# Kernel optimization log

Hardware: AMD Instinct MI355X
Metric: run time of the kernel (lower is better)

Reference implementation:

```python
import math
import jax, jax.numpy as jnp
import numpy as np

N_IMAGES = 32
TOTAL_Q = 2048
TOTAL_KV = 2048
Q_IN = 1024
KV_IN = Q_IN + 9
D_QK = 1024
D_V = 1024
N_HEADS = 16
TEMP = 1.0
SCALER = 1.0 / (TEMP * math.sqrt(D_QK // N_HEADS))


def _ragged_seg_ids(total, n_seg, seed):
    rng = np.random.default_rng(seed)
    lens = rng.multinomial(total - n_seg, np.ones(n_seg) / n_seg) + 1  # every segment nonempty
    return jnp.asarray(np.repeat(np.arange(n_seg), lens), dtype=jnp.int32)


def setup_inputs() -> dict:
    key = jax.random.key(0)
    ks = jax.random.split(key, 12)
    s = 0.02
    return {
        "A": jax.random.normal(ks[0], (TOTAL_Q, Q_IN), jnp.float32),
        "B0": jax.random.normal(ks[1], (TOTAL_KV, KV_IN), jnp.float32),
        "seg_q": _ragged_seg_ids(TOTAL_Q, N_IMAGES, 1),
        "seg_kv": _ragged_seg_ids(TOTAL_KV, N_IMAGES, 2),
        "Wq": jax.random.normal(ks[2], (Q_IN, D_QK), jnp.float32) * s,
        "bq": jax.random.normal(ks[3], (D_QK,), jnp.float32) * s,
        "Wk": jax.random.normal(ks[4], (KV_IN, D_QK), jnp.float32) * s,
        "bk": jax.random.normal(ks[5], (D_QK,), jnp.float32) * s,
        "Wv": jax.random.normal(ks[6], (KV_IN, D_V), jnp.float32) * s,
        "bv": jax.random.normal(ks[7], (D_V,), jnp.float32) * s,
        "Wf": jax.random.normal(ks[8], (D_V, Q_IN), jnp.float32) * s,
        "bf": jax.random.normal(ks[9], (Q_IN,), jnp.float32) * s,
    }


def reference(A, B0, seg_q, seg_kv, Wq, bq, Wk, bk, Wv, bv, Wf, bf):
    # Linear projections on packed rows
    q = (A @ Wq + bq).reshape(TOTAL_Q, N_HEADS, -1)     # [Nq, h, dqk]
    k = (B0 @ Wk + bk).reshape(TOTAL_KV, N_HEADS, -1)   # [Nk, h, dqk]
    v = (B0 @ Wv + bv).reshape(TOTAL_KV, N_HEADS, -1)   # [Nk, h, dv]
    # Per-segment attention expressed as a block mask (same math as the
    # original Python loop over splits)
    scores = jnp.einsum('ihd,khd->ihk', q, k) * SCALER  # [Nq, h, Nk]
    mask = (seg_q[:, None] == seg_kv[None, :])[:, None, :]  # [Nq, 1, Nk]
    neg = jnp.finfo(scores.dtype).min
    w = jax.nn.softmax(jnp.where(mask, scores, neg), axis=-1)
    wv = jnp.einsum('ihk,khd->ihd', w, v).reshape(TOTAL_Q, -1)  # [Nq, h*dv]
    return wv @ Wf + bf  # [Nq, q_in_dim]
```

## Files before the change

### kernel.cpp

```cpp
#include <hip/hip_runtime.h>
#include <hip/hip_bf16.h>
#include <math.h>

#define TOTAL_Q   2048
#define TOTAL_KV  2048
#define QIN       1024
#define KVIN      1033
#define KVIN_P    1056
#define DQK       1024
#define DV        1024
#define KVSTR     2048
#define SCALER    0.125f

typedef __bf16 bf16x8 __attribute__((ext_vector_type(8)));
typedef float  f32x4  __attribute__((ext_vector_type(4)));

__device__ __forceinline__ void glds16(const __hip_bfloat16* g, __bf16* l)
{
    __builtin_amdgcn_global_load_lds(
        (const __attribute__((address_space(1))) void*)g,
        (__attribute__((address_space(3))) void*)l,
        16, 0, 0);
}

__global__ __launch_bounds__(256)
void cast_bf16_k(const float* __restrict__ in, __hip_bfloat16* __restrict__ out, int n)
{
    int i = (blockIdx.x * 256 + threadIdx.x) * 4;
    if (i >= n) return;
    float4 f = *(const float4*)(in + i);
    __hip_bfloat16 o[4] = { __float2bfloat16(f.x), __float2bfloat16(f.y),
                            __float2bfloat16(f.z), __float2bfloat16(f.w) };
    *(uint2*)(out + i) = *(const uint2*)o;
}

__global__ __launch_bounds__(256)
void cast_pad_k(const float* __restrict__ in, __hip_bfloat16* __restrict__ out)
{
    int idx = blockIdx.x * 256 + threadIdx.x;
    if (idx >= TOTAL_KV * KVIN_P) return;
    int r = idx / KVIN_P, c = idx - r * KVIN_P;
    float v = (c < KVIN) ? in[(size_t)r * KVIN + c] : 0.f;
    out[idx] = __float2bfloat16(v);
}

__global__ __launch_bounds__(256)
void transpose_cast2_k(const float* __restrict__ W0, const float* __restrict__ W1,
                       __hip_bfloat16* __restrict__ D0, __hip_bfloat16* __restrict__ D1,
                       int K, int Kp)
{
    const float* W = blockIdx.z ? W1 : W0;
    __hip_bfloat16* Wt = blockIdx.z ? D1 : D0;
    __shared__ float tile[32][33];
    const int k0 = blockIdx.x * 32, n0 = blockIdx.y * 32;
    #pragma unroll
    for (int i = 0; i < 4; ++i) {
        int k = k0 + threadIdx.y + i * 8;
        tile[threadIdx.y + i * 8][threadIdx.x] =
            (k < K) ? W[(size_t)k * 1024 + n0 + threadIdx.x] : 0.f;
    }
    __syncthreads();
    #pragma unroll
    for (int i = 0; i < 4; ++i) {
        int n = n0 + threadIdx.y + i * 8;
        Wt[(size_t)n * Kp + k0 + threadIdx.x] =
            __float2bfloat16(tile[threadIdx.x][threadIdx.y + i * 8]);
    }
}

template<int OUT_BF16>
__global__ __launch_bounds__(256)
void gemm_glds(const __hip_bfloat16* __restrict__ A,
               const __hip_bfloat16* __restrict__ Bt,
               const float* __restrict__ biasA, const float* __restrict__ biasB,
               int nsplit,
               void* __restrict__ Cv,
               int M, int N, int K)
{
    __shared__ __bf16 As[128 * 32];
    __shared__ __bf16 Bs[64 * 32];

    const int tid  = threadIdx.x;
    const int wave = tid >> 6, lane = tid & 63;
    const int quad = lane >> 4, l16 = lane & 15;
    const int wm = (wave >> 1) * 64;
    const int wn = (wave & 1) * 32;
    const int row0 = blockIdx.y * 128, col0 = blockIdx.x * 64;

    const int cr = lane >> 2;
    const int cc = (lane & 3) * 8;

    const __hip_bfloat16* ga0 = A  + (size_t)(row0 + (wave * 2 + 0) * 16 + cr) * K + cc;
    const __hip_bfloat16* ga1 = A  + (size_t)(row0 + (wave * 2 + 1) * 16 + cr) * K + cc;
    const __hip_bfloat16* gb0 = Bt + (size_t)(col0 + wave * 16 + cr) * K + cc;

    f32x4 acc[4][2] = {};

    for (int k0 = 0; k0 < K; k0 += 32) {
        glds16(ga0 + k0, &As[(wave * 2 + 0) * 512]);
        glds16(ga1 + k0, &As[(wave * 2 + 1) * 512]);
        glds16(gb0 + k0, &Bs[wave * 512]);
        __syncthreads();

        bf16x8 af[4], bfr[2];
        #pragma unroll
        for (int mi = 0; mi < 4; ++mi)
            af[mi] = *(const bf16x8*)&As[(wm + mi * 16 + l16) * 32 + quad * 8];
        #pragma unroll
        for (int ni = 0; ni < 2; ++ni)
            bfr[ni] = *(const bf16x8*)&Bs[(wn + ni * 16 + l16) * 32 + quad * 8];

        #pragma unroll
        for (int mi = 0; mi < 4; ++mi)
            #pragma unroll
            for (int ni = 0; ni < 2; ++ni)
                acc[mi][ni] = __builtin_amdgcn_mfma_f32_16x16x32_bf16(
                    af[mi], bfr[ni], acc[mi][ni], 0, 0, 0);
        __syncthreads();
    }

    #pragma unroll
    for (int mi = 0; mi < 4; ++mi) {
        #pragma unroll
        for (int ni = 0; ni < 2; ++ni) {
            const int col = col0 + wn + ni * 16 + l16;
            const float b = (col < nsplit) ? biasA[col] : biasB[col - nsplit];
            #pragma unroll
            for (int r = 0; r < 4; ++r) {
                const int row = row0 + wm + mi * 16 + quad * 4 + r;
                const float val = acc[mi][ni][r] + b;
                if (OUT_BF16)
                    ((__hip_bfloat16*)Cv)[(size_t)row * N + col] = __float2bfloat16(val);
                else
                    ((float*)Cv)[(size_t)row * N + col] = val;
            }
        }
    }
}

#define CH 64

__global__ __launch_bounds__(256)
void attn_mfma(const __hip_bfloat16* __restrict__ qg,
               const __hip_bfloat16* __restrict__ kg,
               const __hip_bfloat16* __restrict__ vg,
               const int* __restrict__ seg_q, const int* __restrict__ seg_kv,
               __hip_bfloat16* __restrict__ wv)
{
    const int h = blockIdx.x & 15;
    const int s = blockIdx.x >> 4;

    __shared__ int sb[4];
    __shared__ __bf16 Ks[CH][72];
    __shared__ __bf16 Vt[64][CH + 8];
    __shared__ __bf16 Ps[4][16][CH + 8];

    if (threadIdx.x == 0) {
        int lo, hi;
        lo = 0; hi = TOTAL_Q;
        while (lo < hi) { int m = (lo + hi) >> 1; if (seg_q[m] <  s) lo = m + 1; else hi = m; }
        sb[0] = lo;
        hi = TOTAL_Q;
        while (lo < hi) { int m = (lo + hi) >> 1; if (seg_q[m] <= s) lo = m + 1; else hi = m; }
        sb[1] = lo;
        lo = 0; hi = TOTAL_KV;
        while (lo < hi) { int m = (lo + hi) >> 1; if (seg_kv[m] <  s) lo = m + 1; else hi = m; }
        sb[2] = lo;
        hi = TOTAL_KV;
        while (lo < hi) { int m = (lo + hi) >> 1; if (seg_kv[m] <= s) lo = m + 1; else hi = m; }
        sb[3] = lo;
    }
    __syncthreads();
    const int qbeg = sb[0], qend = sb[1], kbeg = sb[2], kend = sb[3];

    const int tid  = threadIdx.x;
    const int wave = tid >> 6, lane = tid & 63;
    const int quad = lane >> 4, l16 = lane & 15;

    for (int qt = qbeg; qt < qend; qt += 64) {
        const int qrow = qt + wave * 16 + l16;
        const int qrc  = min(qrow, qend - 1);
        bf16x8 qf[2];
        qf[0] = *(const bf16x8*)(qg + (size_t)qrc * DQK + h * 64 + quad * 8);
        qf[1] = *(const bf16x8*)(qg + (size_t)qrc * DQK + h * 64 + 32 + quad * 8);

        float m[4]  = { -1e30f, -1e30f, -1e30f, -1e30f };
        float l[4]  = { 0.f, 0.f, 0.f, 0.f };
        f32x4 acc[4] = {};

        for (int c0 = kbeg; c0 < kend; c0 += CH) {
            const int cl = min(CH, kend - c0);
            __syncthreads();

            #pragma unroll
            for (int it = 0; it < 2; ++it) {
                int e = (it * 256 + tid) * 8;
                int r = e >> 6, d = e & 63;
                bf16x8 z = {};
                if (r < cl)
                    z = *(const bf16x8*)(kg + (size_t)(c0 + r) * KVSTR + h * 64 + d);
                *(bf16x8*)&Ks[r][d] = z;
            }
            #pragma unroll
            for (int it = 0; it < 4; ++it) {
                int e = (it * 256 + tid) * 4;
                int r = e >> 6, d = e & 63;
                __bf16 t0 = 0, t1 = 0, t2 = 0, t3 = 0;
                if (r < cl) {
                    bf16x8 vv;
                    uint2 uu = *(const uint2*)(vg + (size_t)(c0 + r) * KVSTR + h * 64 + d);
                    *(uint2*)&vv = uu;
                    t0 = vv[0]; t1 = vv[1]; t2 = vv[2]; t3 = vv[3];
                }
                Vt[d + 0][r] = t0; Vt[d + 1][r] = t1;
                Vt[d + 2][r] = t2; Vt[d + 3][r] = t3;
            }
            __syncthreads();

            f32x4 sc[4];
            #pragma unroll
            for (int t = 0; t < 4; ++t) {
                bf16x8 b0 = *(const bf16x8*)&Ks[t * 16 + l16][quad * 8];
                bf16x8 b1 = *(const bf16x8*)&Ks[t * 16 + l16][32 + quad * 8];
                f32x4 z = {};
                z = __builtin_amdgcn_mfma_f32_16x16x32_bf16(qf[0], b0, z, 0, 0, 0);
                z = __builtin_amdgcn_mfma_f32_16x16x32_bf16(qf[1], b1, z, 0, 0, 0);
                sc[t] = z;
            }

            float sv[4][4];
            #pragma unroll
            for (int t = 0; t < 4; ++t) {
                const bool ok = (c0 + t * 16 + l16) < kend;
                #pragma unroll
                for (int r = 0; r < 4; ++r)
                    sv[t][r] = ok ? sc[t][r] * SCALER : -1e30f;
            }

            #pragma unroll
            for (int r = 0; r < 4; ++r) {
                float mx = fmaxf(fmaxf(sv[0][r], sv[1][r]), fmaxf(sv[2][r], sv[3][r]));
                mx = fmaxf(mx, __shfl_xor(mx, 1));
                mx = fmaxf(mx, __shfl_xor(mx, 2));
                mx = fmaxf(mx, __shfl_xor(mx, 4));
                mx = fmaxf(mx, __shfl_xor(mx, 8));
                const float mn = fmaxf(m[r], mx);
                const float alpha = __expf(m[r] - mn);
                m[r] = mn;
                float rs = 0.f;
                #pragma unroll
                for (int t = 0; t < 4; ++t) {
                    const float p = __expf(sv[t][r] - mn);
                    sv[t][r] = p;
                    rs += p;
                }
                rs += __shfl_xor(rs, 1);
                rs += __shfl_xor(rs, 2);
                rs += __shfl_xor(rs, 4);
                rs += __shfl_xor(rs, 8);
                l[r] = l[r] * alpha + rs;
                #pragma unroll
                for (int dt = 0; dt < 4; ++dt) acc[dt][r] *= alpha;
            }

            #pragma unroll
            for (int t = 0; t < 4; ++t)
                #pragma unroll
                for (int r = 0; r < 4; ++r)
                    Ps[wave][quad * 4 + r][t * 16 + l16] = (__bf16)sv[t][r];
            __syncthreads();

            #pragma unroll
            for (int ks = 0; ks < 2; ++ks) {
                bf16x8 pa = *(const bf16x8*)&Ps[wave][l16][ks * 32 + quad * 8];
                #pragma unroll
                for (int dt = 0; dt < 4; ++dt) {
                    bf16x8 vbf = *(const bf16x8*)&Vt[dt * 16 + l16][ks * 32 + quad * 8];
                    acc[dt] = __builtin_amdgcn_mfma_f32_16x16x32_bf16(pa, vbf, acc[dt], 0, 0, 0);
                }
            }
        }

        float inv[4];
        #pragma unroll
        for (int r = 0; r < 4; ++r) inv[r] = 1.f / l[r];
        #pragma unroll
        for (int dt = 0; dt < 4; ++dt) {
            #pragma unroll
            for (int r = 0; r < 4; ++r) {
                const int row = qt + wave * 16 + quad * 4 + r;
                if (row < qend)
                    wv[(size_t)row * DV + h * 64 + dt * 16 + l16] =
                        __float2bfloat16(acc[dt][r] * inv[r]);
            }
        }
    }
}

extern "C" void kernel_launch(void* const* d_in, const int* in_sizes, int n_in,
                              void* d_out, int out_size, void* d_ws, size_t ws_size,
                              hipStream_t stream)
{
    const float* A     = (const float*)d_in[0];
    const float* B0    = (const float*)d_in[1];
    const int*   seg_q = (const int*)  d_in[2];
    const int*   seg_kv= (const int*)  d_in[3];
    const float* Wq    = (const float*)d_in[4];
    const float* bq    = (const float*)d_in[5];
    const float* Wk    = (const float*)d_in[6];
    const float* bk    = (const float*)d_in[7];
    const float* Wv    = (const float*)d_in[8];
    const float* bv    = (const float*)d_in[9];
    const float* Wf    = (const float*)d_in[10];
    const float* bf    = (const float*)d_in[11];
    float* out = (float*)d_out;

    __hip_bfloat16* B0bf = (__hip_bfloat16*)d_ws;
    __hip_bfloat16* Wqt  = B0bf + (size_t)TOTAL_KV * KVIN_P;
    __hip_bfloat16* Wkt  = Wqt  + (size_t)QIN * DQK;
    __hip_bfloat16* Wvt  = Wkt  + (size_t)DQK * KVIN_P;
    __hip_bfloat16* Wft  = Wvt  + (size_t)DV * KVIN_P;
    __hip_bfloat16* Abf  = Wft  + (size_t)DV * QIN;
    __hip_bfloat16* qb   = Abf  + (size_t)TOTAL_Q * QIN;
    __hip_bfloat16* kvb  = qb   + (size_t)TOTAL_Q * DQK;
    __hip_bfloat16* wvb  = Abf;

    const dim3 b256(256);

    cast_bf16_k<<<dim3((TOTAL_Q * QIN / 4 + 255) / 256), b256, 0, stream>>>(A, Abf, TOTAL_Q * QIN);
    cast_pad_k<<<dim3((TOTAL_KV * KVIN_P + 255) / 256), b256, 0, stream>>>(B0, B0bf);
    transpose_cast2_k<<<dim3(DQK / 32, 1024 / 32, 2), dim3(32, 8), 0, stream>>>(
        Wq, Wf, Wqt, Wft, QIN, DQK);
    transpose_cast2_k<<<dim3(KVIN_P / 32, 1024 / 32, 2), dim3(32, 8), 0, stream>>>(
        Wk, Wv, Wkt, Wvt, KVIN, KVIN_P);

    gemm_glds<1><<<dim3(DQK / 64, TOTAL_Q / 128), b256, 0, stream>>>(
        Abf, Wqt, bq, bq, DQK, qb, TOTAL_Q, DQK, QIN);
    gemm_glds<1><<<dim3(KVSTR / 64, TOTAL_KV / 128), b256, 0, stream>>>(
        B0bf, Wkt, bk, bv, 1024, kvb, TOTAL_KV, KVSTR, KVIN_P);

    attn_mfma<<<dim3(32 * 16), b256, 0, stream>>>(qb, kvb, kvb + 1024, seg_q, seg_kv, wvb);

    gemm_glds<0><<<dim3(QIN / 64, TOTAL_Q / 128), b256, 0, stream>>>(
        wvb, Wft, bf, bf, QIN, out, TOTAL_Q, QIN, DV);
}
```

Measured before the change: 185.0 us.

## Fuse preprocessing kernels into one launch and merge Q/KV GEMMs with larger tiles

Merges the four cast/transpose kernels into a single prep kernel that dispatches on block index, and folds the Q and KV projection GEMMs into one launch. The merged GEMM uses 128x128 tiles instead of 128x64, so each block reuses more data per load. The B0 cast now writes four elements per thread. This cuts launch overhead and tail gaps between small kernels, but the larger tiles mean fewer blocks (384) and more accumulator registers per thread, which may lower occupancy.

Result: faster. 173.5 us (-6.2%).

```diff
diff --git a/kernel.cpp b/kernel.cpp
--- a/kernel.cpp
+++ b/kernel.cpp
@@ -24,58 +24,160 @@
 }
 
 __global__ __launch_bounds__(256)
-void cast_bf16_k(const float* __restrict__ in, __hip_bfloat16* __restrict__ out, int n)
-{
-    int i = (blockIdx.x * 256 + threadIdx.x) * 4;
-    if (i >= n) return;
-    float4 f = *(const float4*)(in + i);
-    __hip_bfloat16 o[4] = { __float2bfloat16(f.x), __float2bfloat16(f.y),
-                            __float2bfloat16(f.z), __float2bfloat16(f.w) };
-    *(uint2*)(out + i) = *(const uint2*)o;
-}
-
-__global__ __launch_bounds__(256)
-void cast_pad_k(const float* __restrict__ in, __hip_bfloat16* __restrict__ out)
-{
-    int idx = blockIdx.x * 256 + threadIdx.x;
-    if (idx >= TOTAL_KV * KVIN_P) return;
-    int r = idx / KVIN_P, c = idx - r * KVIN_P;
-    float v = (c < KVIN) ? in[(size_t)r * KVIN + c] : 0.f;
-    out[idx] = __float2bfloat16(v);
-}
-
-__global__ __launch_bounds__(256)
-void transpose_cast2_k(const float* __restrict__ W0, const float* __restrict__ W1,
-                       __hip_bfloat16* __restrict__ D0, __hip_bfloat16* __restrict__ D1,
-                       int K, int Kp)
-{
-    const float* W = blockIdx.z ? W1 : W0;
-    __hip_bfloat16* Wt = blockIdx.z ? D1 : D0;
+void prep_k(const float* __restrict__ A,  const float* __restrict__ B0,
+            const float* __restrict__ Wq, const float* __restrict__ Wk,
+            const float* __restrict__ Wv, const float* __restrict__ Wf,
+            __hip_bfloat16* __restrict__ Abf, __hip_bfloat16* __restrict__ B0bf,
+            __hip_bfloat16* __restrict__ Wqt, __hip_bfloat16* __restrict__ Wkt,
+            __hip_bfloat16* __restrict__ Wvt, __hip_bfloat16* __restrict__ Wft)
+{
+    const int b   = blockIdx.x;
+    const int tid = threadIdx.x;
+
+    if (b < 2048) {
+        int i = (b * 256 + tid) * 4;
+        float4 f = *(const float4*)(A + i);
+        __hip_bfloat16 o[4] = { __float2bfloat16(f.x), __float2bfloat16(f.y),
+                                __float2bfloat16(f.z), __float2bfloat16(f.w) };
+        *(uint2*)(Abf + i) = *(const uint2*)o;
+        return;
+    }
+    if (b < 4160) {
+        int idx = ((b - 2048) * 256 + tid) * 4;
+        int r = idx / KVIN_P, c = idx - r * KVIN_P;
+        __hip_bfloat16 o[4];
+        #pragma unroll
+        for (int j = 0; j < 4; ++j)
+            o[j] = __float2bfloat16((c + j < KVIN) ? B0[(size_t)r * KVIN + c + j] : 0.f);
+        *(uint2*)(B0bf + idx) = *(const uint2*)o;
+        return;
+    }
+
+    const float* W; __hip_bfloat16* Wt; int K, Kp, k0, n0;
+    if (b < 6208) {
+        int z = b - 4160;
+        W  = (z >= 1024) ? Wf : Wq;
+        Wt = (z >= 1024) ? Wft : Wqt;
+        K = 1024; Kp = 1024;
+        int rem = z & 1023;
+        k0 = (rem & 31) * 32; n0 = (rem >> 5) * 32;
+    } else {
+        int z = b - 6208;
+        W  = (z >= 1056) ? Wv : Wk;
+        Wt = (z >= 1056) ? Wvt : Wkt;
+        K = KVIN; Kp = KVIN_P;
+        int rem = (z >= 1056) ? z - 1056 : z;
+        k0 = (rem % 33) * 32; n0 = (rem / 33) * 32;
+    }
+    const int tx = tid & 31, ty = tid >> 5;
     __shared__ float tile[32][33];
-    const int k0 = blockIdx.x * 32, n0 = blockIdx.y * 32;
     #pragma unroll
     for (int i = 0; i < 4; ++i) {
-        int k = k0 + threadIdx.y + i * 8;
-        tile[threadIdx.y + i * 8][threadIdx.x] =
-            (k < K) ? W[(size_t)k * 1024 + n0 + threadIdx.x] : 0.f;
+        int k = k0 + ty + i * 8;
+        tile[ty + i * 8][tx] = (k < K) ? W[(size_t)k * 1024 + n0 + tx] : 0.f;
     }
     __syncthreads();
     #pragma unroll
     for (int i = 0; i < 4; ++i) {
-        int n = n0 + threadIdx.y + i * 8;
-        Wt[(size_t)n * Kp + k0 + threadIdx.x] =
-            __float2bfloat16(tile[threadIdx.x][threadIdx.y + i * 8]);
-    }
-}
-
-template<int OUT_BF16>
+        int n = n0 + ty + i * 8;
+        Wt[(size_t)n * Kp + k0 + tx] = __float2bfloat16(tile[tx][ty + i * 8]);
+    }
+}
+
 __global__ __launch_bounds__(256)
-void gemm_glds(const __hip_bfloat16* __restrict__ A,
-               const __hip_bfloat16* __restrict__ Bt,
-               const float* __restrict__ biasA, const float* __restrict__ biasB,
-               int nsplit,
-               void* __restrict__ Cv,
-               int M, int N, int K)
+void gemm_qkv(const __hip_bfloat16* __restrict__ Abf,
+              const __hip_bfloat16* __restrict__ Wqt,
+              const float* __restrict__ bq,
+              __hip_bfloat16* __restrict__ qb,
+              const __hip_bfloat16* __restrict__ B0bf,
+              const __hip_bfloat16* __restrict__ Wkvt,
+              const float* __restrict__ bk, const float* __restrict__ bv,
+              __hip_bfloat16* __restrict__ kvb)
+{
+    __shared__ __bf16 As[128 * 32];
+    __shared__ __bf16 Bs[128 * 32];
+
+    int b = blockIdx.x;
+    const __hip_bfloat16 *Ag, *Btg; const float *bias0, *bias1;
+    __hip_bfloat16* C; int N, K, bx, by;
+    if (b < 128) {
+        Ag = Abf; Btg = Wqt; bias0 = bq; bias1 = bq; C = qb;
+        N = 1024; K = 1024; bx = b & 7; by = b >> 3;
+    } else {
+        b -= 128;
+        Ag = B0bf; Btg = Wkvt; bias0 = bk; bias1 = bv; C = kvb;
+        N = 2048; K = KVIN_P; bx = b & 15; by = b >> 4;
+    }
+    const int row0 = by * 128, col0 = bx * 128;
+
+    const int tid  = threadIdx.x;
+    const int wave = tid >> 6, lane = tid & 63;
+    const int quad = lane >> 4, l16 = lane & 15;
+    const int wm = (wave >> 1) * 64, wn = (wave & 1) * 64;
+
+    const int cr = lane >> 2;
+    const int cc = (lane & 3) * 8;
+
+    const __hip_bfloat16* gsrc[4];
+    __bf16* ldst[4];
+    #pragma unroll
+    for (int i = 0; i < 4; ++i) {
+        int c = wave * 4 + i;
+        if (c < 8) {
+            gsrc[i] = Ag  + (size_t)(row0 + c * 16 + cr) * K + cc;
+            ldst[i] = &As[c * 512];
+        } else {
+            gsrc[i] = Btg + (size_t)(col0 + (c - 8) * 16 + cr) * K + cc;
+            ldst[i] = &Bs[(c - 8) * 512];
+        }
+    }
+
+    f32x4 acc[4][4] = {};
+
+    for (int k0 = 0; k0 < K; k0 += 32) {
+        #pragma unroll
+        for (int i = 0; i < 4; ++i)
+            glds16(gsrc[i] + k0, ldst[i]);
+        __syncthreads();
+
+        bf16x8 af[4], bfr[4];
+        #pragma unroll
+        for (int mi = 0; mi < 4; ++mi)
+            af[mi] = *(const bf16x8*)&As[(wm + mi * 16 + l16) * 32 + quad * 8];
+        #pragma unroll
+        for (int ni = 0; ni < 4; ++ni)
+            bfr[ni] = *(const bf16x8*)&Bs[(wn + ni * 16 + l16) * 32 + quad * 8];
+
+        #pragma unroll
+        for (int mi = 0; mi < 4; ++mi)
+            #pragma unroll
+            for (int ni = 0; ni < 4; ++ni)
+                acc[mi][ni] = __builtin_amdgcn_mfma_f32_16x16x32_bf16(
+                    af[mi], bfr[ni], acc[mi][ni], 0, 0, 0);
+        __syncthreads();
+    }
+
+    #pragma unroll
+    for (int mi = 0; mi < 4; ++mi) {
+        #pragma unroll
+        for (int ni = 0; ni < 4; ++ni) {
+            const int col = col0 + wn + ni * 16 + l16;
+            const float bia = (col < 1024) ? bias0[col] : bias1[col - 1024];
+            #pragma unroll
+            for (int r = 0; r < 4; ++r) {
+                const int row = row0 + wm + mi * 16 + quad * 4 + r;
+                C[(size_t)row * N + col] = __float2bfloat16(acc[mi][ni][r] + bia);
+            }
+        }
+    }
+}
+
+__global__ __launch_bounds__(256)
+void gemm_out(const __hip_bfloat16* __restrict__ A,
+              const __hip_bfloat16* __restrict__ Bt,
+              const float* __restrict__ bias,
+              float* __restrict__ C,
+              int M, int N, int K)
 {
     __shared__ __bf16 As[128 * 32];
     __shared__ __bf16 Bs[64 * 32];
@@ -124,15 +226,11 @@
         #pragma unroll
         for (int ni = 0; ni < 2; ++ni) {
             const int col = col0 + wn + ni * 16 + l16;
-            const float b = (col < nsplit) ? biasA[col] : biasB[col - nsplit];
+            const float b = bias[col];
             #pragma unroll
             for (int r = 0; r < 4; ++r) {
                 const int row = row0 + wm + mi * 16 + quad * 4 + r;
-                const float val = acc[mi][ni][r] + b;
-                if (OUT_BF16)
-                    ((__hip_bfloat16*)Cv)[(size_t)row * N + col] = __float2bfloat16(val);
-                else
-                    ((float*)Cv)[(size_t)row * N + col] = val;
+                C[(size_t)row * N + col] = acc[mi][ni][r] + b;
             }
         }
     }
@@ -327,20 +425,14 @@
 
     const dim3 b256(256);
 
-    cast_bf16_k<<<dim3((TOTAL_Q * QIN / 4 + 255) / 256), b256, 0, stream>>>(A, Abf, TOTAL_Q * QIN);
-    cast_pad_k<<<dim3((TOTAL_KV * KVIN_P + 255) / 256), b256, 0, stream>>>(B0, B0bf);
-    transpose_cast2_k<<<dim3(DQK / 32, 1024 / 32, 2), dim3(32, 8), 0, stream>>>(
-        Wq, Wf, Wqt, Wft, QIN, DQK);
-    transpose_cast2_k<<<dim3(KVIN_P / 32, 1024 / 32, 2), dim3(32, 8), 0, stream>>>(
-        Wk, Wv, Wkt, Wvt, KVIN, KVIN_P);
-
-    gemm_glds<1><<<dim3(DQK / 64, TOTAL_Q / 128), b256, 0, stream>>>(
-        Abf, Wqt, bq, bq, DQK, qb, TOTAL_Q, DQK, QIN);
-    gemm_glds<1><<<dim3(KVSTR / 64, TOTAL_KV / 128), b256, 0, stream>>>(
-        B0bf, Wkt, bk, bv, 1024, kvb, TOTAL_KV, KVSTR, KVIN_P);
+    prep_k<<<dim3(8320), b256, 0, stream>>>(A, B0, Wq, Wk, Wv, Wf,
+                                            Abf, B0bf, Wqt, Wkt, Wvt, Wft);
+
+    gemm_qkv<<<dim3(384), b256, 0, stream>>>(Abf, Wqt, bq, qb,
+                                             B0bf, Wkt, bk, bv, kvb);
 
     attn_mfma<<<dim3(32 * 16), b256, 0, stream>>>(qb, kvb, kvb + 1024, seg_q, seg_kv, wvb);
 
-    gemm_glds<0><<<dim3(QIN / 64, TOTAL_Q / 128), b256, 0, stream>>>(
-        wvb, Wft, bf, bf, QIN, out, TOTAL_Q, QIN, DV);
-}
+    gemm_out<<<dim3(QIN / 64, TOTAL_Q / 128), b256, 0, stream>>>(
+        wvb, Wft, bf, out, TOTAL_Q, QIN, DV);
+}
```
